# Kernel tuning notes

Measured on AMD Instinct MI355X. Metric: run time of the kernel, lower is better.

The kernel has to match this reference:

```python
import jax, jax.numpy as jnp
import numpy as np

N_HOPS = 2
N_ENTITIES = 100000
EMB = 64
N_REL = 32
N_EDGES = 1000000


def _l2norm(x, eps=1e-12):
    # torch F.normalize: x / max(||x||_2, eps) per row
    n = jnp.sqrt(jnp.sum(x * x, axis=1, keepdims=True))
    return x / jnp.maximum(n, eps)


def setup_inputs() -> dict:
    key = jax.random.key(0)
    k1, k2, k3, k4, k5, k6 = jax.random.split(key, 6)
    return {
        "entity_emb": jax.random.normal(k1, (N_ENTITIES, EMB), dtype=jnp.float32),
        "edge_emb": jax.random.normal(k2, (N_REL, EMB), dtype=jnp.float32) * 0.1,
        "q_w": jax.random.normal(k3, (EMB, EMB), dtype=jnp.float32) * (1.0 / np.sqrt(EMB)),
        "k_w": jax.random.normal(k4, (EMB, EMB), dtype=jnp.float32) * (1.0 / np.sqrt(EMB)),
        "edge_index": jax.random.randint(k5, (2, N_EDGES), 0, N_ENTITIES, dtype=jnp.int32),
        "edge_type": jax.random.randint(k6, (N_EDGES,), 0, N_REL, dtype=jnp.int32),
        "mess_dropout": 0,
    }


def reference(entity_emb, edge_emb, q_w, k_w, edge_index, edge_type, mess_dropout):
    head = edge_index[0]
    tail = edge_index[1]
    rel = edge_emb[edge_type]                      # [E, D]
    kg = jnp.zeros_like(entity_emb)
    agg = entity_emb
    for _ in range(N_HOPS):
        # edge-wise tanh attention score
        left = (agg @ q_w)[head]                   # [E, D] (factor GEMM out of gather)
        right = jnp.tanh((rel * agg[tail]) @ k_w)  # [E, D]
        att = jnp.sum(left * right, axis=1)        # [E]
        # scatter_softmax over head segments
        m = jax.ops.segment_max(att, head, num_segments=N_ENTITIES)
        e = jnp.exp(att - jax.lax.stop_gradient(m)[head])
        denom = jax.ops.segment_sum(e, head, num_segments=N_ENTITIES)
        w = e / denom[head]                        # [E]
        # weighted messages + scatter_mean aggregation
        msg = w[:, None] * rel * agg[tail]         # [E, D]
        s = jax.ops.segment_sum(msg, head, num_segments=N_ENTITIES)
        cnt = jax.ops.segment_sum(jnp.ones_like(w), head, num_segments=N_ENTITIES)
        agg = s / jnp.maximum(cnt, 1.0)[:, None]
        # mess_dropout=False path; normalize + residual accumulation
        agg = _l2norm(agg)
        kg = kg + agg + entity_emb
    return kg
```

## Files before the change

kernel.cpp:

```cpp
#include <hip/hip_runtime.h>
#include <math.h>

#define EMB 64
#define MAXREL 32

typedef short bf16x8 __attribute__((ext_vector_type(8)));
typedef float f32x4 __attribute__((ext_vector_type(4)));

__device__ __forceinline__ short f2bf(float f) {
    unsigned u = __float_as_uint(f);
    u += 0x7FFFu + ((u >> 16) & 1u);
    return (short)(u >> 16);
}

#if __has_builtin(__builtin_amdgcn_cvt_pk_bf16_f32)
__device__ __forceinline__ short2 cvt2(float a, float b) {
    return __builtin_bit_cast(short2, __builtin_amdgcn_cvt_pk_bf16_f32(a, b));
}
#else
__device__ __forceinline__ short2 cvt2(float a, float b) {
    return make_short2(f2bf(a), f2bf(b));
}
#endif

__device__ __forceinline__ float lo_bf(unsigned d) { return __uint_as_float(d << 16); }
__device__ __forceinline__ float hi_bf(unsigned d) { return __uint_as_float(d & 0xffff0000u); }
__device__ __forceinline__ float bfs(short s) {
    return __uint_as_float(((unsigned)(unsigned short)s) << 16);
}

__device__ __forceinline__ bf16x8 pack8bf(uint4 U, float4 r0, float4 r1) {
    short2 c0 = cvt2(lo_bf(U.x) * r0.x, hi_bf(U.x) * r0.y);
    short2 c1 = cvt2(lo_bf(U.y) * r0.z, hi_bf(U.y) * r0.w);
    short2 c2 = cvt2(lo_bf(U.z) * r1.x, hi_bf(U.z) * r1.y);
    short2 c3 = cvt2(lo_bf(U.w) * r1.z, hi_bf(U.w) * r1.w);
    bf16x8 a;
    a[0] = c0.x; a[1] = c0.y; a[2] = c1.x; a[3] = c1.y;
    a[4] = c2.x; a[5] = c2.y; a[6] = c3.x; a[7] = c3.y;
    return a;
}

__device__ __forceinline__ float fast_tanh(float x) {
    float ax = fabsf(x);
    float z = __expf(2.0f * ax);
    float r = 1.0f - 2.0f / (z + 1.0f);
    return copysignf(r, x);
}

__global__ void init_kernel(short4* __restrict__ aggbf, float4* __restrict__ kg,
                            const float4* __restrict__ ent, int n4) {
    int i = blockIdx.x * blockDim.x + threadIdx.x;
    if (i < n4) {
        float4 v = ent[i];
        short2 c0 = cvt2(v.x, v.y), c1 = cvt2(v.z, v.w);
        aggbf[i] = make_short4(c0.x, c0.y, c1.x, c1.y);
        kg[i] = make_float4(0.f, 0.f, 0.f, 0.f);
    }
}


__global__ void hist_kernel(int* __restrict__ deg, const int* __restrict__ head, int E) {
    int e = blockIdx.x * blockDim.x + threadIdx.x;
    if (e < E) atomicAdd(&deg[head[e]], 1);
}

__global__ void scan_blocks(const int* __restrict__ deg, int* __restrict__ excl,
                            int* __restrict__ bsum, int n) {
    __shared__ int wsum[4];
    int base = blockIdx.x * 1024;
    int t = threadIdx.x;
    int lane = t & 63, wid = t >> 6;
    int idx = base + t * 4;
    int v0 = (idx + 0 < n) ? deg[idx + 0] : 0;
    int v1 = (idx + 1 < n) ? deg[idx + 1] : 0;
    int v2 = (idx + 2 < n) ? deg[idx + 2] : 0;
    int v3 = (idx + 3 < n) ? deg[idx + 3] : 0;
    int s0 = v0, s1 = s0 + v1, s2 = s1 + v2, s3 = s2 + v3;
    int tsum = s3;
    int inc = tsum;
#pragma unroll
    for (int o = 1; o < 64; o <<= 1) { int u = __shfl_up(inc, o, 64); if (lane >= o) inc += u; }
    if (lane == 63) wsum[wid] = inc;
    __syncthreads();
    int woff = 0;
#pragma unroll
    for (int w = 0; w < 4; ++w) if (w < wid) woff += wsum[w];
    int texcl = woff + inc - tsum;
    if (idx + 0 < n) excl[idx + 0] = texcl;
    if (idx + 1 < n) excl[idx + 1] = texcl + s0;
    if (idx + 2 < n) excl[idx + 2] = texcl + s1;
    if (idx + 3 < n) excl[idx + 3] = texcl + s2;
    if (t == 255) bsum[blockIdx.x] = woff + inc;
}

__global__ void scan_sums(int* __restrict__ bsum, int* __restrict__ excl, int nb, int n, int E) {
    int acc = 0;
    for (int b = 0; b < nb; ++b) { int v = bsum[b]; bsum[b] = acc; acc += v; }
    excl[n] = E;
}

__global__ void scan_add(int* __restrict__ excl, const int* __restrict__ bsum, int n) {
    int i = blockIdx.x * blockDim.x + threadIdx.x;
    if (i < n) excl[i] += bsum[i >> 10];
}

__global__ void sort_scatter(const int* __restrict__ head, const int* __restrict__ tail,
                             const int* __restrict__ etype, const int* __restrict__ offsets,
                             int* __restrict__ cursor, int2* __restrict__ spair, int E) {
    int e = blockIdx.x * blockDim.x + threadIdx.x;
    if (e >= E) return;
    int h = head[e];
    int pos = offsets[h] + atomicAdd(&cursor[h], 1);
    spair[pos] = make_int2(h, tail[e] | (etype[e] << 20));
}


__device__ __forceinline__ void build_bfrags(bf16x8 bfrag[2][4], const float* __restrict__ W,
                                             int lane) {
    int koff = (lane >> 4) * 8;
    int n = lane & 15;
#pragma unroll
    for (int kh = 0; kh < 2; ++kh)
#pragma unroll
        for (int nt = 0; nt < 4; ++nt) {
            bf16x8 b;
#pragma unroll
            for (int j = 0; j < 8; ++j)
                b[j] = f2bf(W[(kh * 32 + koff + j) * EMB + nt * 16 + n]);
            bfrag[kh][nt] = b;
        }
}

__global__ void qproj_mfma_kernel(short* __restrict__ Qbf, const short* __restrict__ aggbf,
                                  const float* __restrict__ qw, int N) {
    int lane = threadIdx.x & 63;
    int gwave = blockIdx.x * (blockDim.x >> 6) + (threadIdx.x >> 6);
    int nwaves = gridDim.x * (blockDim.x >> 6);
    int row = lane & 15;
    int g = lane >> 4;
    int koff = g * 8;

    bf16x8 bfrag[2][4];
    build_bfrags(bfrag, qw, lane);

    int ntiles = (N + 15) >> 4;
    for (int tile = gwave; tile < ntiles; tile += nwaves) {
        int rIdx = min(tile * 16 + row, N - 1);
        const short* rowp = aggbf + (size_t)rIdx * EMB;
        bf16x8 a0 = *(const bf16x8*)(rowp + koff);
        bf16x8 a1 = *(const bf16x8*)(rowp + 32 + koff);
#pragma unroll
        for (int nt = 0; nt < 4; ++nt) {
            f32x4 acc = {0.f, 0.f, 0.f, 0.f};
            acc = __builtin_amdgcn_mfma_f32_16x16x32_bf16(a0, bfrag[0][nt], acc, 0, 0, 0);
            acc = __builtin_amdgcn_mfma_f32_16x16x32_bf16(a1, bfrag[1][nt], acc, 0, 0, 0);
#pragma unroll
            for (int reg = 0; reg < 4; ++reg) {
                int n2 = tile * 16 + g * 4 + reg;
                if (n2 < N) Qbf[(size_t)n2 * EMB + nt * 16 + (lane & 15)] = f2bf(acc[reg]);
            }
        }
    }
}

__global__ void att_mfma_kernel(float* __restrict__ att,
                                const short* __restrict__ aggbf, const short* __restrict__ Qbf,
                                const float* __restrict__ eemb, const float* __restrict__ kw,
                                const int2* __restrict__ spair, int E) {
    int lane = threadIdx.x & 63;
    int gwave = blockIdx.x * (blockDim.x >> 6) + (threadIdx.x >> 6);
    int nwaves = gridDim.x * (blockDim.x >> 6);
    int row = lane & 15;
    int g = lane >> 4;

    bf16x8 bfrag[2][4];
    build_bfrags(bfrag, kw, lane);

    int ntiles = (E + 15) >> 4;
    for (int tile = gwave; tile < ntiles; tile += nwaves) {
        int eld = min(tile * 16 + row, E - 1);
        int2 pr = spair[eld];
        int h = pr.x;
        int t = pr.y & 0xFFFFF;
        unsigned r = ((unsigned)pr.y) >> 20;
        const uint4* rowa = (const uint4*)(aggbf + (size_t)t * EMB);
        const float4* rl4 = (const float4*)(eemb + (size_t)r * EMB);
        uint4 U0 = rowa[g];
        uint4 U1 = rowa[4 + g];
        float4 y0 = rl4[g * 2], y1 = rl4[g * 2 + 1];
        float4 y2 = rl4[8 + g * 2], y3 = rl4[8 + g * 2 + 1];
        bf16x8 a0 = pack8bf(U0, y0, y1);
        bf16x8 a1 = pack8bf(U1, y2, y3);

        float sums0 = 0.f, sums1 = 0.f, sums2 = 0.f, sums3 = 0.f;
#pragma unroll
        for (int nt = 0; nt < 4; ++nt) {
            f32x4 acc = {0.f, 0.f, 0.f, 0.f};
            acc = __builtin_amdgcn_mfma_f32_16x16x32_bf16(a0, bfrag[0][nt], acc, 0, 0, 0);
            acc = __builtin_amdgcn_mfma_f32_16x16x32_bf16(a1, bfrag[1][nt], acc, 0, 0, 0);
#pragma unroll
            for (int reg = 0; reg < 4; ++reg) {
                int row2 = g * 4 + reg;
                int h2 = __shfl(h, row2, 64);
                float q = bfs(Qbf[(size_t)h2 * EMB + nt * 16 + (lane & 15)]);
                float v = q * fast_tanh(acc[reg]);
                if (reg == 0) sums0 += v;
                else if (reg == 1) sums1 += v;
                else if (reg == 2) sums2 += v;
                else sums3 += v;
            }
        }
#pragma unroll
        for (int m = 1; m <= 8; m <<= 1) {
            sums0 += __shfl_xor(sums0, m, 64);
            sums1 += __shfl_xor(sums1, m, 64);
            sums2 += __shfl_xor(sums2, m, 64);
            sums3 += __shfl_xor(sums3, m, 64);
        }
#pragma unroll
        for (int reg = 0; reg < 4; ++reg) {
            int row2 = g * 4 + reg;
            int e2 = tile * 16 + row2;
            float v = (reg == 0) ? sums0 : (reg == 1) ? sums1 : (reg == 2) ? sums2 : sums3;
            if ((lane & 15) == reg && e2 < E) att[e2] = v;
        }
    }
}

__global__ void head_agg_kernel(short* __restrict__ aggNewBf, float* __restrict__ kg,
                                const float* __restrict__ att, const short* __restrict__ aggOldBf,
                                const float* __restrict__ eemb, const float* __restrict__ ent,
                                const int* __restrict__ offsets, const int2* __restrict__ spair,
                                int N, int R) {
    __shared__ float4 elds4[MAXREL * 16];

    int tid = threadIdx.x;
    int lane = tid & 63;
    int wid = tid >> 6;
    int RS = (R < MAXREL) ? R : MAXREL;
    for (int i = tid; i < RS * 16; i += blockDim.x) elds4[i] = ((const float4*)eemb)[i];
    __syncthreads();

    int sub = lane >> 4;
    int q = lane & 15;
    int h = (blockIdx.x * (blockDim.x >> 6) + wid) * 4 + sub;
    if (h >= N) return;
    int beg = offsets[h], end = offsets[h + 1];
    int deg = end - beg;

    float m = -3.4e38f;
    for (int e = beg + q; e < end; e += 16) m = fmaxf(m, att[e]);
#pragma unroll
    for (int o = 1; o <= 8; o <<= 1) m = fmaxf(m, __shfl_xor(m, o, 64));

    float4 acc4 = make_float4(0.f, 0.f, 0.f, 0.f);
    float ssum = 0.f;
    int qbase = lane & 48;
    for (int c = beg; c < end; c += 16) {
        int e = c + q;
        float ev = 0.f; int tr = 0;
        if (e < end) {
            ev = __expf(att[e] - m);
            tr = spair[e].y;
        }
        ssum += ev;
        int nc = min(16, end - c);
        for (int j = 0; j < nc; ++j) {
            int src = qbase | j;
            float ej = __shfl(ev, src, 64);
            int trj = __shfl(tr, src, 64);
            int tj = trj & 0xFFFFF;
            unsigned rj = ((unsigned)trj) >> 20;
            float4 ew = (rj < (unsigned)RS) ? elds4[rj * 16 + q]
                                            : ((const float4*)eemb)[(size_t)rj * 16 + q];
            uint2 X = ((const uint2*)(aggOldBf + (size_t)tj * EMB))[q];
            acc4.x += ej * ew.x * lo_bf(X.x);
            acc4.y += ej * ew.y * hi_bf(X.x);
            acc4.z += ej * ew.z * lo_bf(X.y);
            acc4.w += ej * ew.w * hi_bf(X.y);
        }
    }
#pragma unroll
    for (int o = 1; o <= 8; o <<= 1) ssum += __shfl_xor(ssum, o, 64);

    float scale = (deg > 0) ? 1.0f / (ssum * (float)deg) : 0.f;
    float4 v = make_float4(acc4.x * scale, acc4.y * scale, acc4.z * scale, acc4.w * scale);
    float ss = v.x * v.x + v.y * v.y + v.z * v.z + v.w * v.w;
#pragma unroll
    for (int o = 1; o <= 8; o <<= 1) ss += __shfl_xor(ss, o, 64);
    float rinv = 1.0f / fmaxf(sqrtf(ss), 1e-12f);
    v.x *= rinv; v.y *= rinv; v.z *= rinv; v.w *= rinv;

    short2 c0 = cvt2(v.x, v.y), c1 = cvt2(v.z, v.w);
    ((short4*)aggNewBf)[(size_t)h * 16 + q] = make_short4(c0.x, c0.y, c1.x, c1.y);
    float4 kgv = ((float4*)kg)[(size_t)h * 16 + q];
    float4 ev2 = ((const float4*)ent)[(size_t)h * 16 + q];
    kgv.x += v.x + ev2.x; kgv.y += v.y + ev2.y;
    kgv.z += v.z + ev2.z; kgv.w += v.w + ev2.w;
    ((float4*)kg)[(size_t)h * 16 + q] = kgv;
}

extern "C" void kernel_launch(void* const* d_in, const int* in_sizes, int n_in,
                              void* d_out, int out_size, void* d_ws, size_t ws_size,
                              hipStream_t stream) {
    const float* ent  = (const float*)d_in[0];
    const float* eemb = (const float*)d_in[1];
    const float* qw   = (const float*)d_in[2];
    const float* kw   = (const float*)d_in[3];
    const int* eidx  = (const int*)d_in[4];
    const int* etype = (const int*)d_in[5];

    const int N = in_sizes[0] / EMB;
    const int R = in_sizes[1] / EMB;
    const int E = in_sizes[5];
    const int* head = eidx;
    const int* tail = eidx + E;

    float* kg = (float*)d_out;

    float* att   = (float*)d_ws;
    int2* spair  = (int2*)(att + E);
    int* offsets = (int*)(spair + E);
    int* deg     = offsets + (N + 1);
    int* cursor  = deg + N;
    int* bsum    = cursor + N;
    uintptr_t pa = ((uintptr_t)(bsum + 1024) + 15) & ~(uintptr_t)15;
    short* aggbf_a = (short*)pa;
    short* aggbf_b = aggbf_a + (size_t)N * EMB;
    short* Qbf     = aggbf_b + (size_t)N * EMB;

    const int NT = 256;
    const int nb = (N + 1023) / 1024;

    init_kernel<<<(N * EMB / 4 + NT - 1) / NT, NT, 0, stream>>>(
        (short4*)aggbf_a, (float4*)kg, (const float4*)ent, N * EMB / 4);
    hipMemsetAsync(deg, 0, (size_t)N * 4, stream);
    hipMemsetAsync(cursor, 0, (size_t)N * 4, stream);
    hist_kernel<<<(E + NT - 1) / NT, NT, 0, stream>>>(deg, head, E);
    scan_blocks<<<nb, NT, 0, stream>>>(deg, offsets, bsum, N);
    scan_sums<<<1, 1, 0, stream>>>(bsum, offsets, nb, N, E);
    scan_add<<<(N + NT - 1) / NT, NT, 0, stream>>>(offsets, bsum, N);
    sort_scatter<<<(E + NT - 1) / NT, NT, 0, stream>>>(head, tail, etype, offsets, cursor,
                                                       spair, E);

    short* curbf = aggbf_a;
    short* nxtbf = aggbf_b;
    for (int hop = 0; hop < 2; ++hop) {
        qproj_mfma_kernel<<<512, NT, 0, stream>>>(Qbf, curbf, qw, N);
        att_mfma_kernel<<<1024, NT, 0, stream>>>(att, curbf, Qbf, eemb, kw, spair, E);
        head_agg_kernel<<<(N + 15) / 16, NT, 0, stream>>>(nxtbf, kg, att, curbf,
                                                          eemb, ent, offsets, spair, N, R);
        short* ts = curbf; curbf = nxtbf; nxtbf = ts;
    }
}
```

Before: 457.4 us.

## Replace atomic edge scatter with two-level bucket sort and tweak scans and kernels

Replaces the per-edge global-atomic counting-sort scatter with a two-pass bucket sort. Block-local shared-memory counting first scatters edges into 512-head buckets, then each bucket is sorted in LDS and written out coalesced. The single-thread block-sum scan becomes a parallel wave scan. It also adds a fast reciprocal in tanh, unrolls the full-chunk aggregation loop, and doubles the attention kernel grid. The risks are an extra pass over the edge data, reusing the Q buffer as scratch, and bucket sizes overflowing the LDS capacity, which falls back to uncoalesced writes.

```diff
diff --git a/kernel.cpp b/kernel.cpp
--- a/kernel.cpp
+++ b/kernel.cpp
@@ -3,6 +3,9 @@
 
 #define EMB 64
 #define MAXREL 32
+#define BSHIFT 9
+#define BCAP 6912
+#define CH 2048
 
 typedef short bf16x8 __attribute__((ext_vector_type(8)));
 typedef float f32x4 __attribute__((ext_vector_type(4)));
@@ -40,10 +43,18 @@
     return a;
 }
 
+__device__ __forceinline__ float fast_rcp(float x) {
+#if __has_builtin(__builtin_amdgcn_rcpf)
+    return __builtin_amdgcn_rcpf(x);
+#else
+    return 1.0f / x;
+#endif
+}
+
 __device__ __forceinline__ float fast_tanh(float x) {
     float ax = fabsf(x);
     float z = __expf(2.0f * ax);
-    float r = 1.0f - 2.0f / (z + 1.0f);
+    float r = 1.0f - 2.0f * fast_rcp(z + 1.0f);
     return copysignf(r, x);
 }
 
@@ -94,9 +105,28 @@
 }
 
 __global__ void scan_sums(int* __restrict__ bsum, int* __restrict__ excl, int nb, int n, int E) {
-    int acc = 0;
-    for (int b = 0; b < nb; ++b) { int v = bsum[b]; bsum[b] = acc; acc += v; }
-    excl[n] = E;
+    __shared__ int ws[4];
+    int t = threadIdx.x;
+    if (nb > 256) {
+        if (t == 0) {
+            int acc = 0;
+            for (int b = 0; b < nb; ++b) { int v = bsum[b]; bsum[b] = acc; acc += v; }
+            excl[n] = E;
+        }
+        return;
+    }
+    int lane = t & 63, wid = t >> 6;
+    int v = (t < nb) ? bsum[t] : 0;
+    int inc = v;
+#pragma unroll
+    for (int o = 1; o < 64; o <<= 1) { int u = __shfl_up(inc, o, 64); if (lane >= o) inc += u; }
+    if (lane == 63) ws[wid] = inc;
+    __syncthreads();
+    int woff = 0;
+#pragma unroll
+    for (int w = 0; w < 4; ++w) if (w < wid) woff += ws[w];
+    if (t < nb) bsum[t] = woff + inc - v;
+    if (t == 0) excl[n] = E;
 }
 
 __global__ void scan_add(int* __restrict__ excl, const int* __restrict__ bsum, int n) {
@@ -104,14 +134,77 @@
     if (i < n) excl[i] += bsum[i >> 10];
 }
 
-__global__ void sort_scatter(const int* __restrict__ head, const int* __restrict__ tail,
-                             const int* __restrict__ etype, const int* __restrict__ offsets,
-                             int* __restrict__ cursor, int2* __restrict__ spair, int E) {
-    int e = blockIdx.x * blockDim.x + threadIdx.x;
-    if (e >= E) return;
-    int h = head[e];
-    int pos = offsets[h] + atomicAdd(&cursor[h], 1);
-    spair[pos] = make_int2(h, tail[e] | (etype[e] << 20));
+__global__ void bucket_init(int* __restrict__ bcursor, const int* __restrict__ offsets,
+                            int nb, int N) {
+    int b = blockIdx.x * blockDim.x + threadIdx.x;
+    if (b < nb) bcursor[b] = offsets[min(b << BSHIFT, N)];
+}
+
+__global__ void bucket_scatter(const int* __restrict__ head, const int* __restrict__ tail,
+                               const int* __restrict__ etype, int* __restrict__ bcursor,
+                               int2* __restrict__ tmp, int E, int nb) {
+    __shared__ int lcnt[512];
+    __shared__ int lbase[512];
+    int t = threadIdx.x;
+    int base = blockIdx.x * CH;
+    for (int i = t; i < 512; i += 256) lcnt[i] = 0;
+    __syncthreads();
+    int myh[8];
+#pragma unroll
+    for (int i = 0; i < 8; ++i) {
+        int e = base + i * 256 + t;
+        if (e < E) {
+            int h = head[e];
+            myh[i] = h;
+            atomicAdd(&lcnt[h >> BSHIFT], 1);
+        } else myh[i] = -1;
+    }
+    __syncthreads();
+    for (int b = t; b < nb; b += 256) {
+        int c = lcnt[b];
+        lbase[b] = (c > 0) ? atomicAdd(&bcursor[b], c) : 0;
+        lcnt[b] = 0;
+    }
+    __syncthreads();
+#pragma unroll
+    for (int i = 0; i < 8; ++i) {
+        int e = base + i * 256 + t;
+        if (e < E) {
+            int h = myh[i];
+            int b = h >> BSHIFT;
+            int pos = lbase[b] + atomicAdd(&lcnt[b], 1);
+            tmp[pos] = make_int2(h, tail[e] | (etype[e] << 20));
+        }
+    }
+}
+
+__global__ void bucket_sort(const int* __restrict__ offsets, const int2* __restrict__ tmp,
+                            int2* __restrict__ spair, int N) {
+    __shared__ int2 staged[BCAP];
+    __shared__ int lcur[1 << BSHIFT];
+    int b = blockIdx.x;
+    int h0 = b << BSHIFT;
+    int h1 = min(h0 + (1 << BSHIFT), N);
+    int r0 = offsets[h0], r1 = offsets[h1];
+    int cnt = r1 - r0;
+    int t = threadIdx.x;
+    for (int h = h0 + t; h < h1; h += blockDim.x) lcur[h - h0] = offsets[h] - r0;
+    __syncthreads();
+    if (cnt <= BCAP) {
+        for (int i = t; i < cnt; i += blockDim.x) {
+            int2 rec = tmp[r0 + i];
+            int lp = atomicAdd(&lcur[rec.x - h0], 1);
+            staged[lp] = rec;
+        }
+        __syncthreads();
+        for (int i = t; i < cnt; i += blockDim.x) spair[r0 + i] = staged[i];
+    } else {
+        for (int i = t; i < cnt; i += blockDim.x) {
+            int2 rec = tmp[r0 + i];
+            int lp = atomicAdd(&lcur[rec.x - h0], 1);
+            spair[r0 + lp] = rec;
+        }
+    }
 }
 
 
@@ -265,7 +358,7 @@
         }
         ssum += ev;
         int nc = min(16, end - c);
-        for (int j = 0; j < nc; ++j) {
+        auto body = [&](int j) {
             int src = qbase | j;
             float ej = __shfl(ev, src, 64);
             int trj = __shfl(tr, src, 64);
@@ -278,6 +371,12 @@
             acc4.y += ej * ew.y * hi_bf(X.x);
             acc4.z += ej * ew.z * lo_bf(X.y);
             acc4.w += ej * ew.w * hi_bf(X.y);
+        };
+        if (nc == 16) {
+#pragma unroll 4
+            for (int j = 0; j < 16; ++j) body(j);
+        } else {
+            for (int j = 0; j < nc; ++j) body(j);
         }
     }
 #pragma unroll
@@ -322,32 +421,34 @@
     int2* spair  = (int2*)(att + E);
     int* offsets = (int*)(spair + E);
     int* deg     = offsets + (N + 1);
-    int* cursor  = deg + N;
-    int* bsum    = cursor + N;
+    int* bcursor = deg + N;
+    int* bsum    = bcursor + N;
     uintptr_t pa = ((uintptr_t)(bsum + 1024) + 15) & ~(uintptr_t)15;
     short* aggbf_a = (short*)pa;
     short* aggbf_b = aggbf_a + (size_t)N * EMB;
     short* Qbf     = aggbf_b + (size_t)N * EMB;
+    int2* tmp      = (int2*)Qbf;
 
     const int NT = 256;
     const int nb = (N + 1023) / 1024;
+    const int nbk = (N + (1 << BSHIFT) - 1) >> BSHIFT;
 
     init_kernel<<<(N * EMB / 4 + NT - 1) / NT, NT, 0, stream>>>(
         (short4*)aggbf_a, (float4*)kg, (const float4*)ent, N * EMB / 4);
     hipMemsetAsync(deg, 0, (size_t)N * 4, stream);
-    hipMemsetAsync(cursor, 0, (size_t)N * 4, stream);
     hist_kernel<<<(E + NT - 1) / NT, NT, 0, stream>>>(deg, head, E);
     scan_blocks<<<nb, NT, 0, stream>>>(deg, offsets, bsum, N);
-    scan_sums<<<1, 1, 0, stream>>>(bsum, offsets, nb, N, E);
+    scan_sums<<<1, NT, 0, stream>>>(bsum, offsets, nb, N, E);
     scan_add<<<(N + NT - 1) / NT, NT, 0, stream>>>(offsets, bsum, N);
-    sort_scatter<<<(E + NT - 1) / NT, NT, 0, stream>>>(head, tail, etype, offsets, cursor,
-                                                       spair, E);
+    bucket_init<<<(nbk + NT - 1) / NT, NT, 0, stream>>>(bcursor, offsets, nbk, N);
+    bucket_scatter<<<(E + CH - 1) / CH, NT, 0, stream>>>(head, tail, etype, bcursor, tmp, E, nbk);
+    bucket_sort<<<nbk, NT, 0, stream>>>(offsets, tmp, spair, N);
 
     short* curbf = aggbf_a;
     short* nxtbf = aggbf_b;
     for (int hop = 0; hop < 2; ++hop) {
         qproj_mfma_kernel<<<512, NT, 0, stream>>>(Qbf, curbf, qw, N);
-        att_mfma_kernel<<<1024, NT, 0, stream>>>(att, curbf, Qbf, eemb, kw, spair, E);
+        att_mfma_kernel<<<2048, NT, 0, stream>>>(att, curbf, Qbf, eemb, kw, spair, E);
         head_agg_kernel<<<(N + 15) / 16, NT, 0, stream>>>(nxtbf, kg, att, curbf,
                                                           eemb, ent, offsets, spair, N, R);
         short* ts = curbf; curbf = nxtbf; nxtbf = ts;
```

Measured after the change: 420.0 us. -8.2%, faster.
